# Kernel optimization log

Hardware: AMD Instinct MI355X
Metric: run time of the kernel (lower is better)

The kernel has to match this reference:

```python
import jax, jax.numpy as jnp
import numpy as np

EPS = 1e-8
D = 1024      # embedding_dim
NH = 4        # num_heads
HD = D // NH  # head_dim
B, S = 4, 2048


def setup_inputs() -> dict:
    key = jax.random.key(0)
    k1, k2 = jax.random.split(key)
    x = jax.random.normal(k1, (B, S, 4 * D), dtype=jnp.float32)
    # small-init std = sqrt(2/(5*head_dim)) as in reset_parameters
    std = float(np.sqrt(2.0 / (5.0 * HD)))
    gate_weights = jax.random.normal(k2, (4, NH, HD, HD), dtype=jnp.float32) * std
    # biases: z,i,o zero; f gets powerlaw init (block 0 of 1 -> exponent 0.3)
    term = jnp.arange(HD, dtype=jnp.float32) / (HD - 1.0)
    f_bias = -(-5.0 + 12.0 * term ** 0.3)  # [HD]
    gate_biases = jnp.zeros((4, NH, HD), dtype=jnp.float32)
    gate_biases = gate_biases.at[2].set(jnp.broadcast_to(f_bias, (NH, HD)))
    return {"x_gate_inputs": x, "gate_weights": gate_weights, "gate_biases": gate_biases}


def _slstm_forward(x, W, biases):
    Bn, Sn, _ = x.shape
    # split into 4 gate pre-activations and apply headwise linear per gate
    xg = x.reshape(Bn, Sn, 4, NH, HD)           # gate order z,i,f,o along axis 2
    xg = jnp.moveaxis(xg, 2, 0)                  # [4,B,S,NH,HD]
    # headwise projection: einsum over head-in dim, per gate g and head h
    gates = jnp.einsum('gbshi,ghoi->gbsho', xg, W) + biases[:, None, None]  # [4,B,S,NH,HD]
    gates = jnp.moveaxis(gates, 2, 0)            # [S,4,B,NH,HD] for scan over time

    h0 = jnp.zeros((Bn, NH, HD), dtype=x.dtype)
    carry0 = (h0, h0, h0, jnp.zeros((Bn, NH, HD), dtype=jnp.float32))

    def step(carry, g_t):
        h, c, n, m = carry
        z_b, i_b, f_b, o_b = g_t[0], g_t[1], g_t[2], g_t[3]
        z_val = jnp.tanh(z_b)
        o_val = jax.nn.sigmoid(o_b)
        # faithful to original: exp then log(.+EPS), in m-state dtype (fp32)
        log_f = jnp.log(jnp.exp(f_b).astype(jnp.float32) + EPS)
        log_i = jnp.log(jnp.exp(i_b).astype(jnp.float32) + EPS)
        m_new = jnp.maximum(log_f + m, log_i)
        i_hat = jnp.exp(log_i - m_new).astype(x.dtype)
        f_hat = jnp.exp(log_f + m - m_new).astype(x.dtype)
        c_new = f_hat * c + i_hat * z_val
        n_new = f_hat * n + i_hat
        h_new = o_val * (c_new / (n_new + EPS))
        return (h_new, c_new, n_new, m_new), h_new

    (h_f, c_f, n_f, m_f), hs = jax.lax.scan(step, carry0, gates)
    h_seq = jnp.moveaxis(hs, 0, 1)               # [B,S,NH,HD]
    return h_seq, (h_f, c_f, n_f, m_f)


def reference(x_gate_inputs, gate_weights, gate_biases):
    h_seq, (h_f, c_f, n_f, m_f) = _slstm_forward(x_gate_inputs, gate_weights, gate_biases)
    return h_seq, h_f, c_f, n_f, m_f
```

## Files before the change

### kernel.cpp

```cpp
#include <hip/hip_runtime.h>
#include <cstdint>

#define S_LEN   2048
#define BATCH   4
#define NCH     4096
#define PLANE   ((size_t)S_LEN * NCH)
#define CHUNK   16
#define NCHUNK  128
#define SN      ((size_t)NCHUNK * NCH)
#define EPS     1e-8f

using bf16x8 = __attribute__((ext_vector_type(8))) short;
using f32x4  = __attribute__((ext_vector_type(4))) float;
typedef unsigned short u16;

__device__ __forceinline__ short f2bf(float f) {
  uint32_t u = __builtin_bit_cast(uint32_t, f);
  u += 0x7fffu + ((u >> 16) & 1u);
  return (short)(u >> 16);
}
__device__ __forceinline__ float bf2f(u16 u) {
  return __builtin_bit_cast(float, (uint32_t)u << 16);
}
__device__ __forceinline__ u16 f2h(float f) {
  _Float16 h = (_Float16)f;
  return __builtin_bit_cast(unsigned short, h);
}
__device__ __forceinline__ float h2f(u16 u) {
  return (float)__builtin_bit_cast(_Float16, u);
}

__global__ __launch_bounds__(1024) void gates_gemm6(
    const float* __restrict__ x, const float* __restrict__ W,
    const float* __restrict__ bias,
    u16* __restrict__ gz16, u16* __restrict__ gi16, u16* __restrict__ gf16,
    u16* __restrict__ go16) {
  __shared__ u16 As[2][16 * 264];

  const int gh  = blockIdx.x;
  const int rg  = blockIdx.y;
  const int g   = gh >> 2, hh = gh & 3;
  const int tid = threadIdx.x;
  const int wave = tid >> 6, lane = tid & 63;
  const int l16 = lane & 15, quad = lane >> 4;
  const int n0  = wave * 16;
  const int row0 = rg * 256;

  bf16x8 Bf[8];
  {
    const float* wp = W + ((size_t)gh << 16) + (n0 + l16) * 256 + quad * 8;
#pragma unroll
    for (int kt = 0; kt < 8; ++kt) {
      float4 w0 = *(const float4*)(wp + kt * 32);
      float4 w1 = *(const float4*)(wp + kt * 32 + 4);
      bf16x8 b;
      b[0] = f2bf(w0.x); b[1] = f2bf(w0.y); b[2] = f2bf(w0.z); b[3] = f2bf(w0.w);
      b[4] = f2bf(w1.x); b[5] = f2bf(w1.y); b[6] = f2bf(w1.z); b[7] = f2bf(w1.w);
      Bf[kt] = b;
    }
  }
  const float bv = bias[gh * 256 + n0 + l16];

  const int sr = tid >> 6, sc = tid & 63;
  const float* sbase = x + (size_t)(row0 + sr) * 4096 + g * 1024 + hh * 256 + sc * 4;

  float4 sreg;
  auto gload = [&](int t) { sreg = *(const float4*)(sbase + (size_t)t * 16 * 4096); };
  auto swrite = [&](int buf) {
    ushort4 u;
    u.x = (u16)f2bf(sreg.x); u.y = (u16)f2bf(sreg.y);
    u.z = (u16)f2bf(sreg.z); u.w = (u16)f2bf(sreg.w);
    *(ushort4*)&As[buf][sr * 264 + sc * 4] = u;
  };

  gload(0); swrite(0);
  __syncthreads();

  for (int t = 0; t < 16; ++t) {
    if (t + 1 < 16) gload(t + 1);

    f32x4 acc = (f32x4){0.f, 0.f, 0.f, 0.f};
#pragma unroll
    for (int kt = 0; kt < 8; ++kt) {
      bf16x8 a = *(const bf16x8*)&As[t & 1][l16 * 264 + kt * 32 + quad * 8];
      acc = __builtin_amdgcn_mfma_f32_16x16x32_bf16(a, Bf[kt], acc, 0, 0, 0);
    }

#pragma unroll
    for (int rr = 0; rr < 4; ++rr) {
      int rowi = row0 + t * 16 + quad * 4 + rr;
      int sx = rowi & (S_LEN - 1);
      int bx = rowi >> 11;
      size_t idx = (size_t)sx * NCH + bx * 1024 + hh * 256 + n0 + l16;
      float v = acc[rr] + bv;
      if (g == 1)      gi16[idx] = f2h(v);
      else if (g == 2) gf16[idx] = f2h(v);
      else if (g == 0) {
        float tz = 1.f - 2.f * __builtin_amdgcn_rcpf(1.f + __expf(2.f * v));
        gz16[idx] = (u16)f2bf(tz);
      } else {
        float s = __builtin_amdgcn_rcpf(1.f + __expf(-v));
        go16[idx] = (u16)f2bf(s);
      }
    }

    if (t + 1 < 16) {
      swrite((t + 1) & 1);
      __syncthreads();
    }
  }
}

__global__ __launch_bounds__(256) void scan_pass1(
    const u16* __restrict__ gz16, const u16* __restrict__ gi16,
    const u16* __restrict__ gf16, float* __restrict__ sums) {
  const int t  = blockIdx.x * 256 + threadIdx.x;
  const int ch = t & (NCH - 1);
  const int ck = t >> 12;
  const size_t base = (size_t)ck * CHUNK * NCH + ch;

  float A = 0.f, Bv = -1e30f, D = 0.f, Dn = 0.f;

  float z0[8], i0[8], f0[8], z1[8], i1[8], f1[8];
#pragma unroll
  for (int j = 0; j < 8; ++j) {
    size_t off = base + (size_t)j * NCH;
    z0[j] = bf2f(gz16[off]); i0[j] = h2f(gi16[off]); f0[j] = h2f(gf16[off]);
  }
#pragma unroll
  for (int j = 0; j < 8; ++j) {
    size_t off = base + (size_t)(8 + j) * NCH;
    z1[j] = bf2f(gz16[off]); i1[j] = h2f(gi16[off]); f1[j] = h2f(gf16[off]);
  }

  auto step = [&](float z, float i, float f) {
    float Bn = fmaxf(Bv + f, i);
    float e1 = __expf(Bv + f - Bn);
    float e2 = __expf(i - Bn);
    D  = e1 * D + e2 * z;
    Dn = e1 * Dn + e2;
    A += f;
    Bv = Bn;
  };

#pragma unroll
  for (int j = 0; j < 8; ++j) step(z0[j], i0[j], f0[j]);
#pragma unroll
  for (int j = 0; j < 8; ++j) step(z1[j], i1[j], f1[j]);

  const size_t idx = (size_t)ck * NCH + ch;
  sums[idx]          = A;
  sums[SN + idx]     = Bv;
  sums[2 * SN + idx] = D;
  sums[3 * SN + idx] = Dn;
}

__global__ __launch_bounds__(256) void scan_pass2(
    const float* __restrict__ sums, float* __restrict__ ent) {
  const int gt   = blockIdx.x * 256 + threadIdx.x;
  const int ch   = gt >> 6;
  const int lane = gt & 63;

  const size_t i0 = (size_t)(2 * lane) * NCH + ch;
  const size_t i1 = (size_t)(2 * lane + 1) * NCH + ch;
  float A0 = sums[i0], B0 = sums[SN + i0], D0 = sums[2 * SN + i0], N0 = sums[3 * SN + i0];
  float A1 = sums[i1], B1 = sums[SN + i1], D1 = sums[2 * SN + i1], N1 = sums[3 * SN + i1];

  float A, B, D, N;
  {
    float Bn = fmaxf(B0 + A1, B1);
    D = __expf(B0 + A1 - Bn) * D0 + __expf(B1 - Bn) * D1;
    N = __expf(B0 + A1 - Bn) * N0 + __expf(B1 - Bn) * N1;
    A = A0 + A1;
    B = Bn;
  }

#pragma unroll
  for (int d = 1; d < 64; d <<= 1) {
    float Ae = __shfl_up(A, d, 64);
    float Be = __shfl_up(B, d, 64);
    float De = __shfl_up(D, d, 64);
    float Ne = __shfl_up(N, d, 64);
    if (lane >= d) {
      float Bn = fmaxf(Be + A, B);
      float e1 = __expf(Be + A - Bn);
      float e2 = __expf(B - Bn);
      D = e1 * De + e2 * D;
      N = e1 * Ne + e2 * N;
      A = A + Ae;
      B = Bn;
    }
  }

  float Ae = __shfl_up(A, 1, 64);
  float Be = __shfl_up(B, 1, 64);
  float De = __shfl_up(D, 1, 64);
  float Ne = __shfl_up(N, 1, 64);
  if (lane == 0) { Ae = 0.f; Be = -1e30f; De = 0.f; Ne = 0.f; }

  {
    float m = fmaxf(Ae, Be);
    float eb = __expf(Be - m);
    ent[i0]          = eb * De;
    ent[SN + i0]     = eb * Ne;
    ent[2 * SN + i0] = m;
  }
  {
    float Bf_ = fmaxf(Be + A0, B0);
    float e1 = __expf(Be + A0 - Bf_);
    float e2 = __expf(B0 - Bf_);
    float Df_ = e1 * De + e2 * D0;
    float Nf_ = e1 * Ne + e2 * N0;
    float Af_ = Ae + A0;
    float m = fmaxf(Af_, Bf_);
    float eb = __expf(Bf_ - m);
    ent[i1]          = eb * Df_;
    ent[SN + i1]     = eb * Nf_;
    ent[2 * SN + i1] = m;
  }
}

__global__ __launch_bounds__(256) void scan_pass3(
    const u16* __restrict__ gz16, const u16* __restrict__ gi16,
    const u16* __restrict__ gf16, const u16* __restrict__ go16,
    const float* __restrict__ ent, float* __restrict__ out) {
  const int t  = blockIdx.x * 256 + threadIdx.x;
  const int ch = t & (NCH - 1);
  const int ck = t >> 12;

  const size_t idx0 = (size_t)ck * NCH + ch;
  float c = ent[idx0];
  float n = ent[SN + idx0];
  float m = ent[2 * SN + idx0];

  const int b = ch >> 10, d = ch & 1023;
  const size_t base = (size_t)ck * CHUNK * NCH + ch;
  float* hout = out + (size_t)b * (S_LEN * 1024) + (size_t)(ck * CHUNK) * 1024 + d;

  float hv = 0.f;
  float z0[8], i0[8], f0[8], o0[8], z1[8], i1[8], f1[8], o1[8];
#pragma unroll
  for (int j = 0; j < 8; ++j) {
    size_t off = base + (size_t)j * NCH;
    z0[j] = bf2f(gz16[off]); i0[j] = h2f(gi16[off]);
    f0[j] = h2f(gf16[off]); o0[j] = bf2f(go16[off]);
  }
#pragma unroll
  for (int j = 0; j < 8; ++j) {
    size_t off = base + (size_t)(8 + j) * NCH;
    z1[j] = bf2f(gz16[off]); i1[j] = h2f(gi16[off]);
    f1[j] = h2f(gf16[off]); o1[j] = bf2f(go16[off]);
  }

  auto step = [&](float z, float i, float f, float o, int s) {
    float mn = fmaxf(f + m, i);
    float fh = __expf(f + m - mn);
    float ih = __expf(i - mn);
    c = fh * c + ih * z;
    n = fh * n + ih;
    m = mn;
    hv = o * c * __builtin_amdgcn_rcpf(n + EPS);
    hout[(size_t)s * 1024] = hv;
  };

#pragma unroll
  for (int j = 0; j < 8; ++j) step(z0[j], i0[j], f0[j], o0[j], j);
#pragma unroll
  for (int j = 0; j < 8; ++j) step(z1[j], i1[j], f1[j], o1[j], 8 + j);

  if (ck == NCHUNK - 1) {
    float* fin = out + (size_t)BATCH * S_LEN * 1024;
    fin[ch]            = hv;
    fin[NCH + ch]      = c;
    fin[2 * NCH + ch]  = n;
    fin[3 * NCH + ch]  = m;
  }
}

extern "C" void kernel_launch(void* const* d_in, const int* in_sizes, int n_in,
                              void* d_out, int out_size, void* d_ws, size_t ws_size,
                              hipStream_t stream) {
  const float* x    = (const float*)d_in[0];
  const float* W    = (const float*)d_in[1];
  const float* bias = (const float*)d_in[2];
  float* out = (float*)d_out;

  u16*   gz16 = (u16*)d_ws;
  u16*   gi16 = gz16 + PLANE;
  u16*   gf16 = gi16 + PLANE;
  u16*   go16 = gf16 + PLANE;
  float* sums = (float*)(go16 + PLANE);
  float* ent  = sums + 4 * SN;

  gates_gemm6<<<dim3(16, 32), dim3(1024), 0, stream>>>(x, W, bias, gz16, gi16, gf16, go16);
  scan_pass1<<<dim3(2048), dim3(256), 0, stream>>>(gz16, gi16, gf16, sums);
  scan_pass2<<<dim3(1024), dim3(256), 0, stream>>>(sums, ent);
  scan_pass3<<<dim3(2048), dim3(256), 0, stream>>>(gz16, gi16, gf16, go16, ent, out);
}
```

Before: 278.4 us.

## Store gate planes chunk-major and double scan chunk length to 32

The GEMM epilogue now writes gate values in a chunk-contiguous layout using 4-wide vector stores. The scan passes then read each thread's 32 timesteps with 16-byte vector loads instead of strided scalar loads. Chunk length doubles, so passes 1 and 3 launch half as many threads and pass 2 handles one chunk per lane. This trades fewer memory instructions for more scattered GEMM stores, less parallelism and a longer serial chain per thread.

```diff
diff --git a/kernel.cpp b/kernel.cpp
--- a/kernel.cpp
+++ b/kernel.cpp
@@ -4,13 +4,14 @@
 #define S_LEN   2048
 #define BATCH   4
 #define NCH     4096
+#define CHUNK   32
+#define NCHUNK  64
 #define PLANE   ((size_t)S_LEN * NCH)
-#define CHUNK   16
-#define NCHUNK  128
 #define SN      ((size_t)NCHUNK * NCH)
 #define EPS     1e-8f
 
 using bf16x8 = __attribute__((ext_vector_type(8))) short;
+using u16x8  = __attribute__((ext_vector_type(8))) unsigned short;
 using f32x4  = __attribute__((ext_vector_type(4))) float;
 typedef unsigned short u16;
 
@@ -30,7 +31,8 @@
   return (float)__builtin_bit_cast(_Float16, u);
 }
 
-__global__ __launch_bounds__(1024) void gates_gemm6(
+
+__global__ __launch_bounds__(1024) void gates_gemm7(
     const float* __restrict__ x, const float* __restrict__ W,
     const float* __restrict__ bias,
     u16* __restrict__ gz16, u16* __restrict__ gi16, u16* __restrict__ gf16,
@@ -86,21 +88,34 @@
       acc = __builtin_amdgcn_mfma_f32_16x16x32_bf16(a, Bf[kt], acc, 0, 0, 0);
     }
 
-#pragma unroll
-    for (int rr = 0; rr < 4; ++rr) {
-      int rowi = row0 + t * 16 + quad * 4 + rr;
-      int sx = rowi & (S_LEN - 1);
-      int bx = rowi >> 11;
-      size_t idx = (size_t)sx * NCH + bx * 1024 + hh * 256 + n0 + l16;
-      float v = acc[rr] + bv;
-      if (g == 1)      gi16[idx] = f2h(v);
-      else if (g == 2) gf16[idx] = f2h(v);
-      else if (g == 0) {
-        float tz = 1.f - 2.f * __builtin_amdgcn_rcpf(1.f + __expf(2.f * v));
-        gz16[idx] = (u16)f2bf(tz);
+    {
+      int rowb = row0 + t * 16 + quad * 4;
+      int sx   = rowb & (S_LEN - 1);
+      int bx   = rowb >> 11;
+      int ck   = sx >> 5, sin = sx & 31;
+      int ch   = bx * 1024 + hh * 256 + n0 + l16;
+      size_t idx = ((size_t)ck * NCH + ch) * CHUNK + sin;
+
+      float v0 = acc[0] + bv, v1 = acc[1] + bv, v2 = acc[2] + bv, v3 = acc[3] + bv;
+      ushort4 uo;
+      if (g == 1) {
+        uo.x = f2h(v0); uo.y = f2h(v1); uo.z = f2h(v2); uo.w = f2h(v3);
+        *(ushort4*)&gi16[idx] = uo;
+      } else if (g == 2) {
+        uo.x = f2h(v0); uo.y = f2h(v1); uo.z = f2h(v2); uo.w = f2h(v3);
+        *(ushort4*)&gf16[idx] = uo;
+      } else if (g == 0) {
+        auto tz = [](float v) {
+          return (u16)f2bf(1.f - 2.f * __builtin_amdgcn_rcpf(1.f + __expf(2.f * v)));
+        };
+        uo.x = tz(v0); uo.y = tz(v1); uo.z = tz(v2); uo.w = tz(v3);
+        *(ushort4*)&gz16[idx] = uo;
       } else {
-        float s = __builtin_amdgcn_rcpf(1.f + __expf(-v));
-        go16[idx] = (u16)f2bf(s);
+        auto sg = [](float v) {
+          return (u16)f2bf(__builtin_amdgcn_rcpf(1.f + __expf(-v)));
+        };
+        uo.x = sg(v0); uo.y = sg(v1); uo.z = sg(v2); uo.w = sg(v3);
+        *(ushort4*)&go16[idx] = uo;
       }
     }
 
@@ -117,21 +132,17 @@
   const int t  = blockIdx.x * 256 + threadIdx.x;
   const int ch = t & (NCH - 1);
   const int ck = t >> 12;
-  const size_t base = (size_t)ck * CHUNK * NCH + ch;
+  const size_t cb = ((size_t)ck * NCH + ch) * CHUNK;
+
+  u16x8 zv[4], iv[4], fv[4];
+#pragma unroll
+  for (int q = 0; q < 4; ++q) zv[q] = *(const u16x8*)(gz16 + cb + q * 8);
+#pragma unroll
+  for (int q = 0; q < 4; ++q) iv[q] = *(const u16x8*)(gi16 + cb + q * 8);
+#pragma unroll
+  for (int q = 0; q < 4; ++q) fv[q] = *(const u16x8*)(gf16 + cb + q * 8);
 
   float A = 0.f, Bv = -1e30f, D = 0.f, Dn = 0.f;
-
-  float z0[8], i0[8], f0[8], z1[8], i1[8], f1[8];
-#pragma unroll
-  for (int j = 0; j < 8; ++j) {
-    size_t off = base + (size_t)j * NCH;
-    z0[j] = bf2f(gz16[off]); i0[j] = h2f(gi16[off]); f0[j] = h2f(gf16[off]);
-  }
-#pragma unroll
-  for (int j = 0; j < 8; ++j) {
-    size_t off = base + (size_t)(8 + j) * NCH;
-    z1[j] = bf2f(gz16[off]); i1[j] = h2f(gi16[off]); f1[j] = h2f(gf16[off]);
-  }
 
   auto step = [&](float z, float i, float f) {
     float Bn = fmaxf(Bv + f, i);
@@ -144,9 +155,10 @@
   };
 
 #pragma unroll
-  for (int j = 0; j < 8; ++j) step(z0[j], i0[j], f0[j]);
-#pragma unroll
-  for (int j = 0; j < 8; ++j) step(z1[j], i1[j], f1[j]);
+  for (int q = 0; q < 4; ++q)
+#pragma unroll
+    for (int j = 0; j < 8; ++j)
+      step(bf2f(zv[q][j]), h2f(iv[q][j]), h2f(fv[q][j]));
 
   const size_t idx = (size_t)ck * NCH + ch;
   sums[idx]          = A;
@@ -161,33 +173,25 @@
   const int ch   = gt >> 6;
   const int lane = gt & 63;
 
-  const size_t i0 = (size_t)(2 * lane) * NCH + ch;
-  const size_t i1 = (size_t)(2 * lane + 1) * NCH + ch;
-  float A0 = sums[i0], B0 = sums[SN + i0], D0 = sums[2 * SN + i0], N0 = sums[3 * SN + i0];
-  float A1 = sums[i1], B1 = sums[SN + i1], D1 = sums[2 * SN + i1], N1 = sums[3 * SN + i1];
-
-  float A, B, D, N;
-  {
-    float Bn = fmaxf(B0 + A1, B1);
-    D = __expf(B0 + A1 - Bn) * D0 + __expf(B1 - Bn) * D1;
-    N = __expf(B0 + A1 - Bn) * N0 + __expf(B1 - Bn) * N1;
-    A = A0 + A1;
-    B = Bn;
-  }
+  const size_t idx = (size_t)lane * NCH + ch;
+  float A = sums[idx];
+  float B = sums[SN + idx];
+  float D = sums[2 * SN + idx];
+  float N = sums[3 * SN + idx];
 
 #pragma unroll
   for (int d = 1; d < 64; d <<= 1) {
-    float Ae = __shfl_up(A, d, 64);
-    float Be = __shfl_up(B, d, 64);
-    float De = __shfl_up(D, d, 64);
-    float Ne = __shfl_up(N, d, 64);
+    float A1 = __shfl_up(A, d, 64);
+    float B1 = __shfl_up(B, d, 64);
+    float D1 = __shfl_up(D, d, 64);
+    float N1 = __shfl_up(N, d, 64);
     if (lane >= d) {
-      float Bn = fmaxf(Be + A, B);
-      float e1 = __expf(Be + A - Bn);
+      float Bn = fmaxf(B1 + A, B);
+      float e1 = __expf(B1 + A - Bn);
       float e2 = __expf(B - Bn);
-      D = e1 * De + e2 * D;
-      N = e1 * Ne + e2 * N;
-      A = A + Ae;
+      D = e1 * D1 + e2 * D;
+      N = e1 * N1 + e2 * N;
+      A = A + A1;
       B = Bn;
     }
   }
@@ -196,28 +200,20 @@
   float Be = __shfl_up(B, 1, 64);
   float De = __shfl_up(D, 1, 64);
   float Ne = __shfl_up(N, 1, 64);
-  if (lane == 0) { Ae = 0.f; Be = -1e30f; De = 0.f; Ne = 0.f; }
-
-  {
-    float m = fmaxf(Ae, Be);
+
+  float c, n, m;
+  if (lane == 0) {
+    c = 0.f; n = 0.f; m = 0.f;
+  } else {
+    m = fmaxf(Ae, Be);
     float eb = __expf(Be - m);
-    ent[i0]          = eb * De;
-    ent[SN + i0]     = eb * Ne;
-    ent[2 * SN + i0] = m;
-  }
-  {
-    float Bf_ = fmaxf(Be + A0, B0);
-    float e1 = __expf(Be + A0 - Bf_);
-    float e2 = __expf(B0 - Bf_);
-    float Df_ = e1 * De + e2 * D0;
-    float Nf_ = e1 * Ne + e2 * N0;
-    float Af_ = Ae + A0;
-    float m = fmaxf(Af_, Bf_);
-    float eb = __expf(Bf_ - m);
-    ent[i1]          = eb * Df_;
-    ent[SN + i1]     = eb * Nf_;
-    ent[2 * SN + i1] = m;
-  }
+    c = eb * De;
+    n = eb * Ne;
+  }
+
+  ent[idx]          = c;
+  ent[SN + idx]     = n;
+  ent[2 * SN + idx] = m;
 }
 
 __global__ __launch_bounds__(256) void scan_pass3(
@@ -227,6 +223,17 @@
   const int t  = blockIdx.x * 256 + threadIdx.x;
   const int ch = t & (NCH - 1);
   const int ck = t >> 12;
+  const size_t cb = ((size_t)ck * NCH + ch) * CHUNK;
+
+  u16x8 zv[4], iv[4], fv[4], ov[4];
+#pragma unroll
+  for (int q = 0; q < 4; ++q) zv[q] = *(const u16x8*)(gz16 + cb + q * 8);
+#pragma unroll
+  for (int q = 0; q < 4; ++q) iv[q] = *(const u16x8*)(gi16 + cb + q * 8);
+#pragma unroll
+  for (int q = 0; q < 4; ++q) fv[q] = *(const u16x8*)(gf16 + cb + q * 8);
+#pragma unroll
+  for (int q = 0; q < 4; ++q) ov[q] = *(const u16x8*)(go16 + cb + q * 8);
 
   const size_t idx0 = (size_t)ck * NCH + ch;
   float c = ent[idx0];
@@ -234,39 +241,27 @@
   float m = ent[2 * SN + idx0];
 
   const int b = ch >> 10, d = ch & 1023;
-  const size_t base = (size_t)ck * CHUNK * NCH + ch;
   float* hout = out + (size_t)b * (S_LEN * 1024) + (size_t)(ck * CHUNK) * 1024 + d;
 
   float hv = 0.f;
-  float z0[8], i0[8], f0[8], o0[8], z1[8], i1[8], f1[8], o1[8];
-#pragma unroll
-  for (int j = 0; j < 8; ++j) {
-    size_t off = base + (size_t)j * NCH;
-    z0[j] = bf2f(gz16[off]); i0[j] = h2f(gi16[off]);
-    f0[j] = h2f(gf16[off]); o0[j] = bf2f(go16[off]);
-  }
-#pragma unroll
-  for (int j = 0; j < 8; ++j) {
-    size_t off = base + (size_t)(8 + j) * NCH;
-    z1[j] = bf2f(gz16[off]); i1[j] = h2f(gi16[off]);
-    f1[j] = h2f(gf16[off]); o1[j] = bf2f(go16[off]);
-  }
-
-  auto step = [&](float z, float i, float f, float o, int s) {
-    float mn = fmaxf(f + m, i);
-    float fh = __expf(f + m - mn);
-    float ih = __expf(i - mn);
-    c = fh * c + ih * z;
-    n = fh * n + ih;
-    m = mn;
-    hv = o * c * __builtin_amdgcn_rcpf(n + EPS);
-    hout[(size_t)s * 1024] = hv;
-  };
-
-#pragma unroll
-  for (int j = 0; j < 8; ++j) step(z0[j], i0[j], f0[j], o0[j], j);
-#pragma unroll
-  for (int j = 0; j < 8; ++j) step(z1[j], i1[j], f1[j], o1[j], 8 + j);
+#pragma unroll
+  for (int q = 0; q < 4; ++q) {
+#pragma unroll
+    for (int j = 0; j < 8; ++j) {
+      float z = bf2f(zv[q][j]);
+      float i = h2f(iv[q][j]);
+      float f = h2f(fv[q][j]);
+      float o = bf2f(ov[q][j]);
+      float mn = fmaxf(f + m, i);
+      float fh = __expf(f + m - mn);
+      float ih = __expf(i - mn);
+      c = fh * c + ih * z;
+      n = fh * n + ih;
+      m = mn;
+      hv = o * c * __builtin_amdgcn_rcpf(n + EPS);
+      hout[(size_t)(q * 8 + j) * 1024] = hv;
+    }
+  }
 
   if (ck == NCHUNK - 1) {
     float* fin = out + (size_t)BATCH * S_LEN * 1024;
@@ -292,8 +287,8 @@
   float* sums = (float*)(go16 + PLANE);
   float* ent  = sums + 4 * SN;
 
-  gates_gemm6<<<dim3(16, 32), dim3(1024), 0, stream>>>(x, W, bias, gz16, gi16, gf16, go16);
-  scan_pass1<<<dim3(2048), dim3(256), 0, stream>>>(gz16, gi16, gf16, sums);
+  gates_gemm7<<<dim3(16, 32), dim3(1024), 0, stream>>>(x, W, bias, gz16, gi16, gf16, go16);
+  scan_pass1<<<dim3(1024), dim3(256), 0, stream>>>(gz16, gi16, gf16, sums);
   scan_pass2<<<dim3(1024), dim3(256), 0, stream>>>(sums, ent);
-  scan_pass3<<<dim3(2048), dim3(256), 0, stream>>>(gz16, gi16, gf16, go16, ent, out);
-}
+  scan_pass3<<<dim3(1024), dim3(256), 0, stream>>>(gz16, gi16, gf16, go16, ent, out);
+}
```

Result: no change. 274.7 us (-1.3%).
